# Kernel tuning notes

Measured on AMD Instinct MI355X. Metric: run time of the kernel, lower is better.

The kernel has to match this reference:

```python
import jax, jax.numpy as jnp
import numpy as np

KS = 3  # kernel_size


def _im2col(x):
    # x: (N, C, H, W) -> (N, H*W, C*KS*KS), matching torch unfold (channel-major,
    # kernel-position-minor) ordering with padding=1.
    N, C, H, W = x.shape
    xp = jnp.pad(x, ((0, 0), (0, 0), (1, 1), (1, 1)))
    patches = jnp.stack(
        [xp[:, :, i:i + H, j:j + W] for i in range(KS) for j in range(KS)],
        axis=2,
    )  # (N, C, 9, H, W)
    return patches.reshape(N, C * KS * KS, H * W).transpose(0, 2, 1)


def setup_inputs() -> dict:
    key = jax.random.key(0)
    k1, k2, k3, k4, k5 = jax.random.split(key, 5)
    N, C, H, W = 4, 64, 192, 192
    outC = 3
    return {
        "lr_features": jax.random.normal(k1, (N, C, H, W), dtype=jnp.float32),
        "W1": jax.random.normal(k2, (3, 256), dtype=jnp.float32) * 0.05,
        "b1": jax.random.normal(k3, (256,), dtype=jnp.float32) * 0.05,
        "W2": jax.random.normal(k4, (256, KS * KS * C * outC), dtype=jnp.float32) * 0.05,
        "b2": jax.random.normal(k5, (KS * KS * C * outC,), dtype=jnp.float32) * 0.05,
        "sr_scale": 4,
    }


def reference(lr_features, W1, b1, W2, b2, sr_scale):
    # Integer sr_scale: mask_mat is all-true and pos_mat_small is the s*s grid
    # of sub-pixel offsets [1/s, i/s, j/s] for i, j in [0, s).
    N, C, H, W = lr_features.shape
    s = int(np.ceil(sr_scale))
    inv = 1.0 / float(sr_scale)
    off = jnp.arange(s, dtype=jnp.float32) * inv
    pos = jnp.stack(jnp.meshgrid(off, off, indexing="ij"), axis=-1).reshape(s * s, 2)
    pos = jnp.concatenate(
        [jnp.full((s * s, 1), inv, dtype=jnp.float32), pos], axis=1
    )  # (s^2, 3)

    # Pos2Weight MLP -> per-subpixel dynamic conv weights (s^2, C*9, outC)
    hidden = jax.nn.relu(pos @ W1 + b1)
    local_weight = (hidden @ W2 + b2).reshape(s * s, KS * KS * C, -1)
    outC = local_weight.shape[-1]

    cols = _im2col(lr_features)  # (N, H*W, C*9)
    # batched small matmul: each sub-pixel position has its own filter
    out = jnp.einsum("npk,sko->nspo", cols, local_weight)  # (N, s^2, H*W, outC)
    out = out.reshape(N, s, s, H, W, outC)
    out = out.transpose(0, 5, 3, 1, 4, 2).reshape(N, outC, s * H, s * W)
    return out
```

## Files before the change

### kernel.cpp

```cpp
#include <hip/hip_runtime.h>


#define HH   192
#define WWD  192
#define SS   4
#define OC   3
#define PO   48
#define HID  256
#define W2LD 1728

typedef short  bf16x8 __attribute__((ext_vector_type(8)));
typedef float  f32x4  __attribute__((ext_vector_type(4)));

static __device__ __forceinline__ short f2bf(float f) {
    unsigned u = __float_as_uint(f);
    unsigned r = (u + 0x7fffu + ((u >> 16) & 1u)) >> 16;
    return (short)r;
}

__global__ __launch_bounds__(256) void lw_kernel(
        const float* __restrict__ W1, const float* __restrict__ b1,
        const float* __restrict__ W2, const float* __restrict__ b2,
        short* __restrict__ lwb) {
    __shared__ float hlds[HID * 16];
    const int tid = threadIdx.x;
    {
        const float w0 = W1[tid], w1 = W1[HID + tid], w2 = W1[2 * HID + tid], bb = b1[tid];
#pragma unroll
        for (int g = 0; g < 4; ++g) {
            float4 hv;
            float* hp = (float*)&hv;
#pragma unroll
            for (int pp = 0; pp < 4; ++pp) {
                const int p = g * 4 + pp;
                const float pi = (float)(p >> 2) * 0.25f;
                const float pj = (float)(p & 3) * 0.25f;
                const float v = 0.25f * w0 + pi * w1 + pj * w2 + bb;
                hp[pp] = v > 0.f ? v : 0.f;
            }
            *(float4*)&hlds[tid * 16 + g * 4] = hv;
        }
    }
    __syncthreads();

    const int col = blockIdx.x * 256 + tid;
    const int pg  = blockIdx.y;
    if (col < W2LD) {
        float a0 = 0.f, a1 = 0.f, a2 = 0.f, a3 = 0.f;
#pragma unroll 16
        for (int h = 0; h < HID; ++h) {
            const float v  = W2[h * W2LD + col];
            const float4 hv = *(const float4*)&hlds[h * 16 + pg * 4];
            a0 += hv.x * v; a1 += hv.y * v; a2 += hv.z * v; a3 += hv.w * v;
        }
        const float bv = b2[col];
        const int o = col % 3, kc = col / 3;
        const int tap = kc % 9, c = kc / 9;
        const int p0 = pg * 4;
        lwb[(tap * PO + (p0 + 0) * 3 + o) * 64 + c] = f2bf(a0 + bv);
        lwb[(tap * PO + (p0 + 1) * 3 + o) * 64 + c] = f2bf(a1 + bv);
        lwb[(tap * PO + (p0 + 2) * 3 + o) * 64 + c] = f2bf(a2 + bv);
        lwb[(tap * PO + (p0 + 3) * 3 + o) * 64 + c] = f2bf(a3 + bv);
    }
}

__global__ __launch_bounds__(192, 3) void meta_up_mfma(
        const float* __restrict__ x, const short* __restrict__ lwb,
        float* __restrict__ out) {
    __shared__ __align__(16) short smem[3 * 66 * 64];
    short* xlds = smem;
    float* obuf = (float*)smem;

    const int strip = (blockIdx.x & 7) * 288 + (blockIdx.x >> 3);
    const int n   = strip / (HH * 3);
    const int rem = strip % (HH * 3);
    const int h   = rem / 3;
    const int wch = rem % 3;
    const int w0  = wch * 64;

    const int tid  = threadIdx.x;
    const int lane = tid & 63, wv = tid >> 6;
    const int quad = lane >> 4, l15 = lane & 15;

    bf16x8 Bfrag[18];
#pragma unroll
    for (int tap = 0; tap < 9; ++tap)
#pragma unroll
        for (int kc2 = 0; kc2 < 2; ++kc2)
            Bfrag[tap * 2 + kc2] = *(const bf16x8*)
                &lwb[(tap * PO + wv * 16 + l15) * 64 + kc2 * 32 + quad * 8];

    {
        const int gr  = h + wv - 1;
        const bool rok = (unsigned)gr < (unsigned)HH;
        const int gc  = w0 - 1 + lane;
        const bool cok = rok && ((unsigned)gc < (unsigned)WWD);
        const float* __restrict__ xr =
            x + ((size_t)n * 64 * HH + (size_t)(rok ? gr : 0)) * WWD + (cok ? gc : 0);
#pragma unroll
        for (int cb = 0; cb < 8; ++cb) {
            bf16x8 pk;
#pragma unroll
            for (int cc = 0; cc < 8; ++cc) {
                const float vv = cok ? xr[(size_t)(cb * 8 + cc) * HH * WWD] : 0.f;
                pk[cc] = f2bf(vv);
            }
            *(bf16x8*)&xlds[(wv * 66 + lane) * 64 + ((cb ^ (lane & 7)) << 3)] = pk;
        }
        if (lane < 16) {
            const int jt = 64 + (lane >> 3);
            const int cb = lane & 7;
            const int gc2 = w0 - 1 + jt;
            const bool cok2 = rok && ((unsigned)gc2 < (unsigned)WWD);
            bf16x8 pk;
#pragma unroll
            for (int cc = 0; cc < 8; ++cc) {
                const float vv = cok2 ?
                    x[((size_t)(n * 64 + cb * 8 + cc) * HH + gr) * WWD + gc2] : 0.f;
                pk[cc] = f2bf(vv);
            }
            *(bf16x8*)&xlds[(wv * 66 + jt) * 64 + ((cb ^ (jt & 7)) << 3)] = pk;
        }
    }
    __syncthreads();

    f32x4 acc[4];
#pragma unroll
    for (int mt = 0; mt < 4; ++mt) acc[mt] = (f32x4){0.f, 0.f, 0.f, 0.f};

#pragma unroll
    for (int tap = 0; tap < 9; ++tap) {
        const int di = tap / 3, dj = tap % 3;
#pragma unroll
        for (int kc2 = 0; kc2 < 2; ++kc2) {
            const bf16x8 b = Bfrag[tap * 2 + kc2];
#pragma unroll
            for (int mt = 0; mt < 4; ++mt) {
                const int col = mt * 16 + l15 + dj;
                const int blk = (kc2 * 4 + quad) ^ (col & 7);
                bf16x8 a = *(const bf16x8*)&xlds[(di * 66 + col) * 64 + (blk << 3)];
                acc[mt] = __builtin_amdgcn_mfma_f32_16x16x32_bf16(a, b, acc[mt], 0, 0, 0);
            }
        }
    }

    __syncthreads();
    {
        const int po = wv * 16 + l15;
        const int o  = po % 3;
        const int p  = po / 3;
        const int si = p >> 2, sj = p & 3;
        const int osi = o * 4 + si;
#pragma unroll
        for (int mt = 0; mt < 4; ++mt)
#pragma unroll
            for (int r4 = 0; r4 < 4; ++r4) {
                const int wl = mt * 16 + quad * 4 + r4;
                obuf[osi * 260 + wl * 4 + sj] = acc[mt][r4];
            }
    }
    __syncthreads();
    {
        const int osi = tid >> 4;
        const int c16 = tid & 15;
        const int o = osi >> 2, si = osi & 3;
        const size_t base =
            ((size_t)(n * OC + o) * (SS * HH) + (size_t)(SS * h + si)) * (SS * WWD)
            + (size_t)(4 * w0) + c16 * 16;
        const float* __restrict__ src = &obuf[osi * 260 + c16 * 16];
#pragma unroll
        for (int i = 0; i < 4; ++i)
            *(float4*)&out[base + i * 4] = *(const float4*)&src[i * 4];
    }
}

extern "C" void kernel_launch(void* const* d_in, const int* in_sizes, int n_in,
                              void* d_out, int out_size, void* d_ws, size_t ws_size,
                              hipStream_t stream) {
    const float* x  = (const float*)d_in[0];
    const float* W1 = (const float*)d_in[1];
    const float* b1 = (const float*)d_in[2];
    const float* W2 = (const float*)d_in[3];
    const float* b2 = (const float*)d_in[4];
    float* out = (float*)d_out;
    short* lwb = (short*)d_ws;

    lw_kernel<<<dim3(7, 4), 256, 0, stream>>>(W1, b1, W2, b2, lwb);
    meta_up_mfma<<<4 * HH * 3, 192, 0, stream>>>(x, lwb, out);
}
```

Baseline: 131.4 us.

## Process four output rows per block to reuse halo rows and weight fragments

```diff
diff --git a/kernel.cpp b/kernel.cpp
--- a/kernel.cpp
+++ b/kernel.cpp
@@ -22,60 +22,43 @@
         const float* __restrict__ W1, const float* __restrict__ b1,
         const float* __restrict__ W2, const float* __restrict__ b2,
         short* __restrict__ lwb) {
-    __shared__ float hlds[HID * 16];
+    __shared__ float hlds[HID];
     const int tid = threadIdx.x;
+    const int p   = blockIdx.y;
     {
-        const float w0 = W1[tid], w1 = W1[HID + tid], w2 = W1[2 * HID + tid], bb = b1[tid];
-#pragma unroll
-        for (int g = 0; g < 4; ++g) {
-            float4 hv;
-            float* hp = (float*)&hv;
-#pragma unroll
-            for (int pp = 0; pp < 4; ++pp) {
-                const int p = g * 4 + pp;
-                const float pi = (float)(p >> 2) * 0.25f;
-                const float pj = (float)(p & 3) * 0.25f;
-                const float v = 0.25f * w0 + pi * w1 + pj * w2 + bb;
-                hp[pp] = v > 0.f ? v : 0.f;
-            }
-            *(float4*)&hlds[tid * 16 + g * 4] = hv;
-        }
+        const float pi = (float)(p >> 2) * 0.25f;
+        const float pj = (float)(p & 3) * 0.25f;
+        const float v = 0.25f * W1[tid] + pi * W1[HID + tid] + pj * W1[2 * HID + tid]
+                      + b1[tid];
+        hlds[tid] = v > 0.f ? v : 0.f;
     }
     __syncthreads();
 
     const int col = blockIdx.x * 256 + tid;
-    const int pg  = blockIdx.y;
     if (col < W2LD) {
-        float a0 = 0.f, a1 = 0.f, a2 = 0.f, a3 = 0.f;
+        float a = 0.f;
 #pragma unroll 16
-        for (int h = 0; h < HID; ++h) {
-            const float v  = W2[h * W2LD + col];
-            const float4 hv = *(const float4*)&hlds[h * 16 + pg * 4];
-            a0 += hv.x * v; a1 += hv.y * v; a2 += hv.z * v; a3 += hv.w * v;
-        }
-        const float bv = b2[col];
+        for (int h = 0; h < HID; ++h)
+            a += hlds[h] * W2[h * W2LD + col];
         const int o = col % 3, kc = col / 3;
         const int tap = kc % 9, c = kc / 9;
-        const int p0 = pg * 4;
-        lwb[(tap * PO + (p0 + 0) * 3 + o) * 64 + c] = f2bf(a0 + bv);
-        lwb[(tap * PO + (p0 + 1) * 3 + o) * 64 + c] = f2bf(a1 + bv);
-        lwb[(tap * PO + (p0 + 2) * 3 + o) * 64 + c] = f2bf(a2 + bv);
-        lwb[(tap * PO + (p0 + 3) * 3 + o) * 64 + c] = f2bf(a3 + bv);
+        lwb[(tap * PO + p * 3 + o) * 64 + c] = f2bf(a + b2[col]);
     }
 }
 
 __global__ __launch_bounds__(192, 3) void meta_up_mfma(
         const float* __restrict__ x, const short* __restrict__ lwb,
         float* __restrict__ out) {
-    __shared__ __align__(16) short smem[3 * 66 * 64];
+    __shared__ __align__(16) short smem[6 * 66 * 64];
     short* xlds = smem;
     float* obuf = (float*)smem;
 
-    const int strip = (blockIdx.x & 7) * 288 + (blockIdx.x >> 3);
-    const int n   = strip / (HH * 3);
-    const int rem = strip % (HH * 3);
-    const int h   = rem / 3;
+    const int tile = (blockIdx.x & 7) * 72 + (blockIdx.x >> 3);
+    const int n   = tile / (48 * 3);
+    const int rem = tile % (48 * 3);
+    const int hb  = rem / 3;
     const int wch = rem % 3;
+    const int h0  = hb * 4;
     const int w0  = wch * 64;
 
     const int tid  = threadIdx.x;
@@ -90,8 +73,10 @@
             Bfrag[tap * 2 + kc2] = *(const bf16x8*)
                 &lwb[(tap * PO + wv * 16 + l15) * 64 + kc2 * 32 + quad * 8];
 
-    {
-        const int gr  = h + wv - 1;
+#pragma unroll
+    for (int rr2 = 0; rr2 < 2; ++rr2) {
+        const int r  = wv * 2 + rr2;
+        const int gr = h0 - 1 + r;
         const bool rok = (unsigned)gr < (unsigned)HH;
         const int gc  = w0 - 1 + lane;
         const bool cok = rok && ((unsigned)gc < (unsigned)WWD);
@@ -105,7 +90,7 @@
                 const float vv = cok ? xr[(size_t)(cb * 8 + cc) * HH * WWD] : 0.f;
                 pk[cc] = f2bf(vv);
             }
-            *(bf16x8*)&xlds[(wv * 66 + lane) * 64 + ((cb ^ (lane & 7)) << 3)] = pk;
+            *(bf16x8*)&xlds[(r * 66 + lane) * 64 + ((cb ^ (lane & 7)) << 3)] = pk;
         }
         if (lane < 16) {
             const int jt = 64 + (lane >> 3);
@@ -119,14 +104,14 @@
                     x[((size_t)(n * 64 + cb * 8 + cc) * HH + gr) * WWD + gc2] : 0.f;
                 pk[cc] = f2bf(vv);
             }
-            *(bf16x8*)&xlds[(wv * 66 + jt) * 64 + ((cb ^ (jt & 7)) << 3)] = pk;
+            *(bf16x8*)&xlds[(r * 66 + jt) * 64 + ((cb ^ (jt & 7)) << 3)] = pk;
         }
     }
     __syncthreads();
 
-    f32x4 acc[4];
+    f32x4 acc[16];
 #pragma unroll
-    for (int mt = 0; mt < 4; ++mt) acc[mt] = (f32x4){0.f, 0.f, 0.f, 0.f};
+    for (int i = 0; i < 16; ++i) acc[i] = (f32x4){0.f, 0.f, 0.f, 0.f};
 
 #pragma unroll
     for (int tap = 0; tap < 9; ++tap) {
@@ -135,11 +120,16 @@
         for (int kc2 = 0; kc2 < 2; ++kc2) {
             const bf16x8 b = Bfrag[tap * 2 + kc2];
 #pragma unroll
-            for (int mt = 0; mt < 4; ++mt) {
-                const int col = mt * 16 + l15 + dj;
-                const int blk = (kc2 * 4 + quad) ^ (col & 7);
-                bf16x8 a = *(const bf16x8*)&xlds[(di * 66 + col) * 64 + (blk << 3)];
-                acc[mt] = __builtin_amdgcn_mfma_f32_16x16x32_bf16(a, b, acc[mt], 0, 0, 0);
+            for (int rr = 0; rr < 4; ++rr) {
+#pragma unroll
+                for (int mt = 0; mt < 4; ++mt) {
+                    const int col = mt * 16 + l15 + dj;
+                    const int blk = (kc2 * 4 + quad) ^ (col & 7);
+                    bf16x8 a = *(const bf16x8*)
+                        &xlds[((rr + di) * 66 + col) * 64 + (blk << 3)];
+                    acc[rr * 4 + mt] =
+                        __builtin_amdgcn_mfma_f32_16x16x32_bf16(a, b, acc[rr * 4 + mt], 0, 0, 0);
+                }
             }
         }
     }
@@ -152,25 +142,30 @@
         const int si = p >> 2, sj = p & 3;
         const int osi = o * 4 + si;
 #pragma unroll
-        for (int mt = 0; mt < 4; ++mt)
+        for (int rr = 0; rr < 4; ++rr)
 #pragma unroll
-            for (int r4 = 0; r4 < 4; ++r4) {
-                const int wl = mt * 16 + quad * 4 + r4;
-                obuf[osi * 260 + wl * 4 + sj] = acc[mt][r4];
-            }
+            for (int mt = 0; mt < 4; ++mt)
+#pragma unroll
+                for (int r4 = 0; r4 < 4; ++r4) {
+                    const int wl = mt * 16 + quad * 4 + r4;
+                    obuf[rr * 3120 + osi * 260 + wl * 4 + sj] = acc[rr * 4 + mt][r4];
+                }
     }
     __syncthreads();
     {
         const int osi = tid >> 4;
         const int c16 = tid & 15;
         const int o = osi >> 2, si = osi & 3;
-        const size_t base =
-            ((size_t)(n * OC + o) * (SS * HH) + (size_t)(SS * h + si)) * (SS * WWD)
-            + (size_t)(4 * w0) + c16 * 16;
-        const float* __restrict__ src = &obuf[osi * 260 + c16 * 16];
 #pragma unroll
-        for (int i = 0; i < 4; ++i)
-            *(float4*)&out[base + i * 4] = *(const float4*)&src[i * 4];
+        for (int rr = 0; rr < 4; ++rr) {
+            const size_t base =
+                ((size_t)(n * OC + o) * (SS * HH) + (size_t)(SS * (h0 + rr) + si)) * (SS * WWD)
+                + (size_t)(4 * w0) + c16 * 16;
+            const float* __restrict__ src = &obuf[rr * 3120 + osi * 260 + c16 * 16];
+#pragma unroll
+            for (int i = 0; i < 4; ++i)
+                *(float4*)&out[base + i * 4] = *(const float4*)&src[i * 4];
+        }
     }
 }
 
@@ -185,6 +180,6 @@
     float* out = (float*)d_out;
     short* lwb = (short*)d_ws;
 
-    lw_kernel<<<dim3(7, 4), 256, 0, stream>>>(W1, b1, W2, b2, lwb);
-    meta_up_mfma<<<4 * HH * 3, 192, 0, stream>>>(x, lwb, out);
+    lw_kernel<<<dim3(7, 16), 256, 0, stream>>>(W1, b1, W2, b2, lwb);
+    meta_up_mfma<<<4 * 48 * 3, 192, 0, stream>>>(x, lwb, out);
 }
```

Measured after the change: 222.6 us. +69.4%, slower.

## Process two output rows per block to share the halo input rows

Applied to the files above, without the earlier changes.

```diff
diff --git a/kernel.cpp b/kernel.cpp
--- a/kernel.cpp
+++ b/kernel.cpp
@@ -47,7 +47,7 @@
     const int pg  = blockIdx.y;
     if (col < W2LD) {
         float a0 = 0.f, a1 = 0.f, a2 = 0.f, a3 = 0.f;
-#pragma unroll 16
+#pragma unroll 32
         for (int h = 0; h < HID; ++h) {
             const float v  = W2[h * W2LD + col];
             const float4 hv = *(const float4*)&hlds[h * 16 + pg * 4];
@@ -64,23 +64,26 @@
     }
 }
 
-__global__ __launch_bounds__(192, 3) void meta_up_mfma(
+__global__ __launch_bounds__(384, 4) void meta_up_mfma(
         const float* __restrict__ x, const short* __restrict__ lwb,
         float* __restrict__ out) {
-    __shared__ __align__(16) short smem[3 * 66 * 64];
+    __shared__ __align__(16) short smem[4 * 66 * 64];
     short* xlds = smem;
     float* obuf = (float*)smem;
 
-    const int strip = (blockIdx.x & 7) * 288 + (blockIdx.x >> 3);
-    const int n   = strip / (HH * 3);
-    const int rem = strip % (HH * 3);
-    const int h   = rem / 3;
+    const int tile = (blockIdx.x & 7) * 144 + (blockIdx.x >> 3);
+    const int n   = tile / (96 * 3);
+    const int rem = tile % (96 * 3);
+    const int hb  = rem / 3;
     const int wch = rem % 3;
+    const int h0  = hb * 2;
     const int w0  = wch * 64;
 
     const int tid  = threadIdx.x;
     const int lane = tid & 63, wv = tid >> 6;
     const int quad = lane >> 4, l15 = lane & 15;
+    const int pt = wv % 3;
+    const int rr = wv / 3;
 
     bf16x8 Bfrag[18];
 #pragma unroll
@@ -88,10 +91,11 @@
 #pragma unroll
         for (int kc2 = 0; kc2 < 2; ++kc2)
             Bfrag[tap * 2 + kc2] = *(const bf16x8*)
-                &lwb[(tap * PO + wv * 16 + l15) * 64 + kc2 * 32 + quad * 8];
+                &lwb[(tap * PO + pt * 16 + l15) * 64 + kc2 * 32 + quad * 8];
 
-    {
-        const int gr  = h + wv - 1;
+    if (wv < 4) {
+        const int r  = wv;
+        const int gr = h0 - 1 + r;
         const bool rok = (unsigned)gr < (unsigned)HH;
         const int gc  = w0 - 1 + lane;
         const bool cok = rok && ((unsigned)gc < (unsigned)WWD);
@@ -105,7 +109,7 @@
                 const float vv = cok ? xr[(size_t)(cb * 8 + cc) * HH * WWD] : 0.f;
                 pk[cc] = f2bf(vv);
             }
-            *(bf16x8*)&xlds[(wv * 66 + lane) * 64 + ((cb ^ (lane & 7)) << 3)] = pk;
+            *(bf16x8*)&xlds[(r * 66 + lane) * 64 + ((cb ^ (lane & 7)) << 3)] = pk;
         }
         if (lane < 16) {
             const int jt = 64 + (lane >> 3);
@@ -119,7 +123,7 @@
                     x[((size_t)(n * 64 + cb * 8 + cc) * HH + gr) * WWD + gc2] : 0.f;
                 pk[cc] = f2bf(vv);
             }
-            *(bf16x8*)&xlds[(wv * 66 + jt) * 64 + ((cb ^ (jt & 7)) << 3)] = pk;
+            *(bf16x8*)&xlds[(r * 66 + jt) * 64 + ((cb ^ (jt & 7)) << 3)] = pk;
         }
     }
     __syncthreads();
@@ -138,7 +142,8 @@
             for (int mt = 0; mt < 4; ++mt) {
                 const int col = mt * 16 + l15 + dj;
                 const int blk = (kc2 * 4 + quad) ^ (col & 7);
-                bf16x8 a = *(const bf16x8*)&xlds[(di * 66 + col) * 64 + (blk << 3)];
+                bf16x8 a = *(const bf16x8*)
+                    &xlds[((rr + di) * 66 + col) * 64 + (blk << 3)];
                 acc[mt] = __builtin_amdgcn_mfma_f32_16x16x32_bf16(a, b, acc[mt], 0, 0, 0);
             }
         }
@@ -146,7 +151,7 @@
 
     __syncthreads();
     {
-        const int po = wv * 16 + l15;
+        const int po = pt * 16 + l15;
         const int o  = po % 3;
         const int p  = po / 3;
         const int si = p >> 2, sj = p & 3;
@@ -156,18 +161,20 @@
 #pragma unroll
             for (int r4 = 0; r4 < 4; ++r4) {
                 const int wl = mt * 16 + quad * 4 + r4;
-                obuf[osi * 260 + wl * 4 + sj] = acc[mt][r4];
+                obuf[rr * 3120 + osi * 260 + wl * 4 + sj] = acc[mt][r4];
             }
     }
     __syncthreads();
     {
-        const int osi = tid >> 4;
-        const int c16 = tid & 15;
+        const int osi2 = tid >> 4;
+        const int c16  = tid & 15;
+        const int rw   = osi2 / 12;
+        const int osi  = osi2 % 12;
         const int o = osi >> 2, si = osi & 3;
         const size_t base =
-            ((size_t)(n * OC + o) * (SS * HH) + (size_t)(SS * h + si)) * (SS * WWD)
+            ((size_t)(n * OC + o) * (SS * HH) + (size_t)(SS * (h0 + rw) + si)) * (SS * WWD)
             + (size_t)(4 * w0) + c16 * 16;
-        const float* __restrict__ src = &obuf[osi * 260 + c16 * 16];
+        const float* __restrict__ src = &obuf[rw * 3120 + osi * 260 + c16 * 16];
 #pragma unroll
         for (int i = 0; i < 4; ++i)
             *(float4*)&out[base + i * 4] = *(const float4*)&src[i * 4];
@@ -186,5 +193,5 @@
     short* lwb = (short*)d_ws;
 
     lw_kernel<<<dim3(7, 4), 256, 0, stream>>>(W1, b1, W2, b2, lwb);
-    meta_up_mfma<<<4 * HH * 3, 192, 0, stream>>>(x, lwb, out);
+    meta_up_mfma<<<4 * 96 * 3, 384, 0, stream>>>(x, lwb, out);
 }
```

Measured after the change: 139.7 us. 6.3% more time.
